# Optimization experiments

Hardware: AMD Instinct MI355X
Metric: run time of the kernel (lower is better)

The kernel has to match this reference:

```python
import jax, jax.numpy as jnp
import numpy as np

# Physical constants of the optics model (angstrom units)
WAVELENGTH = 0.025  # 200 kV electrons
DR = 0.2            # object pixel size
DZ = 10.0           # slice distance
NZ, NY, NX = 8, 512, 512
K = 256
NMODES = 4
M = 128  # detector / probe patch size
EPS = 1e-10


def _propagator_kernel():
    # Fresnel angular-spectrum transfer function, fft-shifted frequency grid
    fy = jnp.fft.fftfreq(M, d=DR).astype(jnp.float32)
    fx = jnp.fft.fftfreq(M, d=DR).astype(jnp.float32)
    f2 = fy[:, None] ** 2 + fx[None, :] ** 2  # (M, M)
    phase = -jnp.pi * WAVELENGTH * DZ * f2
    return jnp.exp(1j * phase.astype(jnp.float32))  # complex64 (M, M)


def setup_inputs() -> dict:
    key = jax.random.key(0)
    k1, k2, k3, k4 = jax.random.split(key, 4)
    V = 0.1 * jax.random.normal(k1, (NZ, NY, NX), dtype=jnp.float32)
    probe_re = jax.random.normal(k2, (NMODES, M, M), dtype=jnp.float32)
    probe_im = jax.random.normal(k3, (NMODES, M, M), dtype=jnp.float32)
    positions = jax.random.randint(k4, (K, 2), 0, NY - M).astype(jnp.int64)
    return {"V": V, "probe_re": probe_re, "probe_im": probe_im, "positions": positions}


def _forward(V, probe_re, probe_im, positions):
    # transmission function per slice: T = exp(i V)  (NZ, NY, NX) complex64
    T = jnp.exp(1j * V)
    pos = positions.astype(jnp.int32)

    # position-indexed crop: (K, NZ, M, M) -> (NZ, K, M, M)
    def crop_one(p):
        return jax.lax.dynamic_slice(T, (jnp.int32(0), p[0], p[1]), (NZ, M, M))

    patches = jax.vmap(crop_one)(pos)            # (K, NZ, M, M)
    patches = jnp.transpose(patches, (1, 0, 2, 3))  # (NZ, K, M, M)

    probe = (probe_re + 1j * probe_im)           # (Nmodes, M, M)
    waves = jnp.broadcast_to(probe[:, None, :, :], (NMODES, K, M, M))

    H = _propagator_kernel()                     # (M, M)

    def step(w, patch):
        w = patch[None] * w                      # transmit through slice
        w = jnp.fft.ifft2(jnp.fft.fft2(w) * H)   # angular-spectrum propagation
        return w, None

    waves, _ = jax.lax.scan(step, waves, patches[:-1])
    waves = waves * patches[-1][None]            # last slice, no propagation after

    # far-field intensity, incoherent sum over probe modes -> amplitudes
    psi_f = jnp.fft.fft2(waves, norm="ortho")    # (Nmodes, K, M, M)
    amp = jnp.sqrt(EPS + jnp.sum(jnp.abs(psi_f) ** 2, axis=0))  # (K, M, M)
    return amp


def reference(V, probe_re, probe_im, positions):
    return _forward(V, probe_re, probe_im, positions)
```

## Files before the change

kernel.cpp:

```cpp
#include <hip/hip_runtime.h>
#include <math.h>

namespace {

constexpr int TNZ = 8, TNY = 512, TNX = 512, TM = 128;
constexpr int PITCH = 129;
constexpr float F0 = 1.0f / (TM * 0.2f);
constexpr float PK = -3.14159265358979323846f * 0.025f * 10.0f;
constexpr float PKF = PK * F0 * F0;
constexpr float INV_N2 = 1.0f / (TM * TM);
constexpr float EPSV = 1e-10f;
constexpr float PIF = 3.14159265358979323846f;
constexpr float RT2H = 0.70710678118654752440f;

typedef float v2 __attribute__((ext_vector_type(2)));
__device__ __forceinline__ v2 mk2(float x, float y) {
  v2 r; r.x = x; r.y = y; return r;
}

template <int I> struct Ic { static constexpr int v = I; };
template <int I, int N, typename F>
__device__ __forceinline__ void u_impl(F&& f) {
  if constexpr (I < N) { f(Ic<I>{}); u_impl<I + 1, N>(f); }
}
template <int N, typename F>
__device__ __forceinline__ void u_for(F&& f) { u_impl<0, N>(f); }

__device__ __forceinline__ v2 cmul(v2 a, v2 b) {
  v2 p = a.xx * b;
  return __builtin_elementwise_fma(mk2(-a.y, a.y), b.yx, p);
}
__device__ __forceinline__ v2 cmulc(v2 a, v2 b) {
  v2 p = a.xx * mk2(b.x, -b.y);
  return __builtin_elementwise_fma(a.yy, b.yx, p);
}
__device__ __forceinline__ v2 fma2(float sg, v2 mine, v2 oth) {
  return __builtin_elementwise_fma(mk2(sg, sg), mine, oth);
}
template <int CTRL>
__device__ __forceinline__ float dppf(float v) {
  return __int_as_float(
      __builtin_amdgcn_mov_dpp(__float_as_int(v), CTRL, 0xF, 0xF, true));
}
template <int M>
__device__ __forceinline__ v2 shdpp(v2 v) {
  constexpr int CTRL = (M == 1) ? 0xB1 : 0x4E;
  return mk2(dppf<CTRL>(v.x), dppf<CTRL>(v.y));
}
template <int M>
__device__ __forceinline__ v2 shswz(v2 v) {
  constexpr int PAT = (M << 10) | 0x1F;
  return mk2(
      __int_as_float(__builtin_amdgcn_ds_swizzle(__float_as_int(v.x), PAT)),
      __int_as_float(__builtin_amdgcn_ds_swizzle(__float_as_int(v.y), PAT)));
}
__device__ __forceinline__ int rev7(int n) {
  return ((n & 1) << 6) | ((n & 2) << 4) | ((n & 4) << 2) | (n & 8) |
         ((n & 16) >> 2) | ((n & 32) >> 4) | ((n & 64) >> 6);
}
constexpr int crev3(int i) { return ((i & 1) << 2) | (i & 2) | ((i & 4) >> 2); }

template <int i> __device__ __forceinline__ v2 mulW8(v2 t) {
  if constexpr (i == 0) return t;
  else if constexpr (i == 1) return (t + mk2(t.y, -t.x)) * RT2H;
  else if constexpr (i == 2) return mk2(t.y, -t.x);
  else return (mk2(t.y, -t.x) - t) * RT2H;
}
template <int i> __device__ __forceinline__ v2 mulW8c(v2 t) {
  if constexpr (i == 0) return t;
  else if constexpr (i == 1) return (t + mk2(-t.y, t.x)) * RT2H;
  else if constexpr (i == 2) return mk2(-t.y, t.x);
  else return (mk2(-t.y, t.x) - t) * RT2H;
}

struct Tw8 {
  v2 wq128, wq64, wq32;
  v2 ws8, ws4, ws2;
  float sg8, sg4, sg2, sg1;
};

__device__ __forceinline__ void dif8(v2 (&X)[8], const Tw8& T) {
  u_for<4>([&](auto I) {
    constexpr int i = I.v;
    v2 A = X[i], B = X[i + 4];
    X[i] = A + B;
    X[i + 4] = mulW8<i>(cmul(A - B, T.wq128));
  });
  u_for<4>([&](auto I) {
    constexpr int g = (I.v >> 1) * 4 + (I.v & 1);
    v2 A = X[g], B = X[g + 2];
    X[g] = A + B;
    v2 d = cmul(A - B, T.wq64);
    X[g + 2] = (g & 1) ? mk2(d.y, -d.x) : d;
  });
  u_for<4>([&](auto I) {
    constexpr int e = I.v * 2;
    v2 A = X[e], B = X[e + 1];
    X[e] = A + B;
    X[e + 1] = cmul(A - B, T.wq32);
  });
  u_for<8>([&](auto I) {
    constexpr int i = I.v;
    v2 o = shswz<8>(X[i]);
    X[i] = cmul(fma2(T.sg8, X[i], o), T.ws8);
  });
  u_for<8>([&](auto I) {
    constexpr int i = I.v;
    v2 o = shswz<4>(X[i]);
    X[i] = cmul(fma2(T.sg4, X[i], o), T.ws4);
  });
  u_for<8>([&](auto I) {
    constexpr int i = I.v;
    v2 o = shdpp<2>(X[i]);
    X[i] = cmul(fma2(T.sg2, X[i], o), T.ws2);
  });
  u_for<8>([&](auto I) {
    constexpr int i = I.v;
    v2 o = shdpp<1>(X[i]);
    X[i] = fma2(T.sg1, X[i], o);
  });
}

__device__ __forceinline__ void dit8(v2 (&X)[8], const Tw8& T) {
  u_for<8>([&](auto I) {
    constexpr int i = I.v;
    v2 o = shdpp<1>(X[i]);
    X[i] = fma2(T.sg1, X[i], o);
  });
  u_for<8>([&](auto I) {
    constexpr int i = I.v;
    v2 u = cmulc(X[i], T.ws2);
    v2 o = shdpp<2>(u);
    X[i] = fma2(T.sg2, u, o);
  });
  u_for<8>([&](auto I) {
    constexpr int i = I.v;
    v2 u = cmulc(X[i], T.ws4);
    v2 o = shswz<4>(u);
    X[i] = fma2(T.sg4, u, o);
  });
  u_for<8>([&](auto I) {
    constexpr int i = I.v;
    v2 u = cmulc(X[i], T.ws8);
    v2 o = shswz<8>(u);
    X[i] = fma2(T.sg8, u, o);
  });
  u_for<4>([&](auto I) {
    constexpr int e = I.v * 2;
    v2 A = X[e];
    v2 t = cmulc(X[e + 1], T.wq32);
    X[e] = A + t;
    X[e + 1] = A - t;
  });
  u_for<4>([&](auto I) {
    constexpr int g = (I.v >> 1) * 4 + (I.v & 1);
    v2 A = X[g];
    v2 t0 = cmulc(X[g + 2], T.wq64);
    v2 t = (g & 1) ? mk2(-t0.y, t0.x) : t0;
    X[g] = A + t;
    X[g + 2] = A - t;
  });
  u_for<4>([&](auto I) {
    constexpr int i = I.v;
    v2 A = X[i];
    v2 t = mulW8c<i>(cmulc(X[i + 4], T.wq128));
    X[i] = A + t;
    X[i + 4] = A - t;
  });
}

template <bool PRE>
__global__ __launch_bounds__(1024)
void msp_mode(const float* __restrict__ V, const v2* __restrict__ Texp,
              const float* __restrict__ Pre, const float* __restrict__ Pim,
              const int* __restrict__ pos, float* __restrict__ out) {
  __shared__ v2 fld[TM * PITCH];
  __shared__ v2 hyb[TM];
  __shared__ v2 hxb[TM];

  const int t = threadIdx.x;
  const int k = blockIdx.x >> 2;
  const int m = blockIdx.x & 3;
  const int q = t & 15;
  const int gg = t >> 4;

  Tw8 T;
  float s, c;
  const float qf = (float)q;
  __sincosf(-PIF * qf / 64.0f, &s, &c);  T.wq128 = mk2(c, s);
  __sincosf(-PIF * qf / 32.0f, &s, &c);  T.wq64  = mk2(c, s);
  __sincosf(-PIF * qf / 16.0f, &s, &c);  T.wq32  = mk2(c, s);
  if (q & 8) { __sincosf(-PIF * (float)(q & 7) / 8.0f, &s, &c); T.ws8 = mk2(c, s); }
  else T.ws8 = mk2(1.f, 0.f);
  if (q & 4) { __sincosf(-PIF * (float)(q & 3) / 4.0f, &s, &c); T.ws4 = mk2(c, s); }
  else T.ws4 = mk2(1.f, 0.f);
  T.ws2 = (q & 2) ? ((q & 1) ? mk2(0.f, -1.f) : mk2(1.f, 0.f)) : mk2(1.f, 0.f);
  T.sg8 = (q & 8) ? -1.f : 1.f;
  T.sg4 = (q & 4) ? -1.f : 1.f;
  T.sg2 = (q & 2) ? -1.f : 1.f;
  T.sg1 = (q & 1) ? -1.f : 1.f;

  const int rev4q =
      ((q & 1) << 3) | ((q & 2) << 1) | ((q & 4) >> 1) | ((q & 8) >> 3);

  if (t < TM) {
    const int qq = t & 15, ii = t >> 4;
    const int r4 = ((qq & 1) << 3) | ((qq & 2) << 1) | ((qq & 4) >> 1) |
                   ((qq & 8) >> 3);
    const int ky = 8 * r4 + crev3(ii);
    const int iy = ky - ((ky & 64) ? 128 : 0);
    float s0, c0;
    __sincosf(PKF * (float)(iy * iy), &s0, &c0);
    hyb[t] = mk2(c0, s0);
    const int kx = rev7(t);
    const int ixf = kx - ((kx & 64) ? 128 : 0);
    __sincosf(PKF * (float)(ixf * ixf), &s0, &c0);
    hxb[t] = mk2(c0 * INV_N2, s0 * INV_N2);
  }

  const int p0 = pos[2 * k];
  const int p1 = pos[2 * k + 1];

#pragma unroll 1
  for (int h = 0; h < 2; ++h) {
    const int y = gg + 64 * h;
    const float* pr = Pre + (m * TM + y) * TM + q;
    const float* pi = Pim + (m * TM + y) * TM + q;
    u_for<8>([&](auto I) {
      constexpr int i = I.v;
      fld[y * PITCH + q + 16 * i] = mk2(pr[16 * i], pi[16 * i]);
    });
  }
  __syncthreads();

#pragma unroll 1
  for (int z = 0; z < TNZ; ++z) {
#pragma unroll 1
    for (int h = 0; h < 2; ++h) {
      const int y = gg + 64 * h;
      v2 X[8];
      u_for<8>([&](auto I) { X[I.v] = fld[y * PITCH + q + 16 * I.v]; });
      if (z > 0) dit8(X, T);
      const int off = ((z * TNY) + (p0 + y)) * TNX + p1 + q;
      if constexpr (PRE) {
        const v2* tb = Texp + off;
        u_for<8>([&](auto I) { X[I.v] = cmul(X[I.v], tb[16 * I.v]); });
      } else {
        const float* vb = V + off;
        u_for<8>([&](auto I) {
          constexpr int i = I.v;
          float v = vb[16 * i];
          float sv, cv;
          __sincosf(v, &sv, &cv);
          X[i] = cmul(X[i], mk2(cv, sv));
        });
      }
      dif8(X, T);
      u_for<8>([&](auto I) { fld[y * PITCH + q + 16 * I.v] = X[I.v]; });
    }
    __syncthreads();

    const bool last = (z == TNZ - 1);
#pragma unroll 1
    for (int h = 0; h < 2; ++h) {
      const int cc = gg + 64 * h;
      v2 X[8];
      u_for<8>([&](auto I) { X[I.v] = fld[(q + 16 * I.v) * PITCH + cc]; });
      dif8(X, T);
      if (!last) {
        const v2 hxv = hxb[cc];
        u_for<8>([&](auto I) {
          constexpr int i = I.v;
          X[i] = cmul(cmul(X[i], hyb[16 * i + q]), hxv);
        });
        dit8(X, T);
        u_for<8>([&](auto I) { fld[(q + 16 * I.v) * PITCH + cc] = X[I.v]; });
      } else {
        float* fldf = reinterpret_cast<float*>(fld);
        const int kxn = rev7(cc) ^ rev4q;
        u_for<8>([&](auto I) {
          constexpr int i = I.v;
          const int ky = 8 * rev4q + crev3(i);
          float v = fmaf(X[i].x, X[i].x, X[i].y * X[i].y);
          fldf[ky * (2 * PITCH) + kxn] = v;
        });
      }
    }
    __syncthreads();
  }

  const float* fldf = reinterpret_cast<const float*>(fld);
  float* ob = out + k * (TM * TM);
#pragma unroll
  for (int ii = 0; ii < 16; ++ii) {
    const int idx = t + 1024 * ii;
    const int ky = idx >> 7, kx = idx & 127;
    const int kxn = kx ^ ((ky >> 3) & 15);
    atomicAdd(&ob[idx], fldf[ky * (2 * PITCH) + kxn]);
  }
}

__global__ __launch_bounds__(256) void texp_k(const float* __restrict__ V,
                                              v2* __restrict__ Texp, int n) {
  const int i = blockIdx.x * 256 + threadIdx.x;
  if (i < n) {
    float s, c;
    __sincosf(V[i], &s, &c);
    Texp[i] = mk2(c, s);
  }
}

__global__ __launch_bounds__(256) void zero_k(float4* __restrict__ p, int n4) {
  const int i = blockIdx.x * 256 + threadIdx.x;
  if (i < n4) p[i] = make_float4(0.f, 0.f, 0.f, 0.f);
}

__global__ __launch_bounds__(256) void sqrt_k(float* __restrict__ p, int n) {
  const int i = blockIdx.x * 256 + threadIdx.x;
  if (i < n) p[i] = sqrtf(EPSV + p[i] * INV_N2);
}

}

extern "C" void kernel_launch(void* const* d_in, const int* in_sizes, int n_in,
                              void* d_out, int out_size, void* d_ws, size_t ws_size,
                              hipStream_t stream) {
  (void)in_sizes; (void)n_in;
  const float* V = (const float*)d_in[0];
  const float* Pre = (const float*)d_in[1];
  const float* Pim = (const float*)d_in[2];
  const int* pos = (const int*)d_in[3];
  float* out = (float*)d_out;
  const int n = out_size;
  const int n4 = n >> 2;
  zero_k<<<dim3((n4 + 255) / 256), dim3(256), 0, stream>>>((float4*)out, n4);

  const int nT = TNZ * TNY * TNX;
  const size_t texp_bytes = (size_t)nT * sizeof(v2);
  if (ws_size >= texp_bytes) {
    v2* Texp = (v2*)d_ws;
    texp_k<<<dim3((nT + 255) / 256), dim3(256), 0, stream>>>(V, Texp, nT);
    msp_mode<true><<<dim3(1024), dim3(1024), 0, stream>>>(V, Texp, Pre, Pim,
                                                          pos, out);
  } else {
    msp_mode<false><<<dim3(1024), dim3(1024), 0, stream>>>(V, nullptr, Pre,
                                                           Pim, pos, out);
  }
  sqrt_k<<<dim3((n + 255) / 256), dim3(256), 0, stream>>>(out, n);
}
```

Measured before the change: 532.3 us.

## Loop probe modes inside one block and fuse zeroing and sqrt epilogue

Each block now handles one scan position and loops over all four probe modes. Far-field intensities are accumulated in per-thread registers instead of being atomically added to global memory. The separate zero-fill and sqrt kernels are removed, and the block writes the final amplitude directly. This cuts two kernel launches, the global atomics and an extra pass over the output. In exchange the grid shrinks from 1024 to 256 blocks, and the 16 accumulator floats add register pressure at 1024 threads per block.

```diff
diff --git a/kernel.cpp b/kernel.cpp
--- a/kernel.cpp
+++ b/kernel.cpp
@@ -171,16 +171,15 @@
 
 template <bool PRE>
 __global__ __launch_bounds__(1024)
-void msp_mode(const float* __restrict__ V, const v2* __restrict__ Texp,
-              const float* __restrict__ Pre, const float* __restrict__ Pim,
-              const int* __restrict__ pos, float* __restrict__ out) {
+void msp_k(const float* __restrict__ V, const v2* __restrict__ Texp,
+           const float* __restrict__ Pre, const float* __restrict__ Pim,
+           const int* __restrict__ pos, float* __restrict__ out) {
   __shared__ v2 fld[TM * PITCH];
   __shared__ v2 hyb[TM];
   __shared__ v2 hxb[TM];
 
   const int t = threadIdx.x;
-  const int k = blockIdx.x >> 2;
-  const int m = blockIdx.x & 3;
+  const int k = blockIdx.x;
   const int q = t & 15;
   const int gg = t >> 4;
 
@@ -221,82 +220,98 @@
   const int p0 = pos[2 * k];
   const int p1 = pos[2 * k + 1];
 
+  v2 acc[8];
+  u_for<8>([&](auto I) { acc[I.v] = mk2(0.f, 0.f); });
+
+#pragma unroll 1
+  for (int m = 0; m < 4; ++m) {
+#pragma unroll 1
+    for (int h = 0; h < 2; ++h) {
+      const int y = gg + 64 * h;
+      const float* pr = Pre + (m * TM + y) * TM + q;
+      const float* pi = Pim + (m * TM + y) * TM + q;
+      u_for<8>([&](auto I) {
+        constexpr int i = I.v;
+        fld[y * PITCH + q + 16 * i] = mk2(pr[16 * i], pi[16 * i]);
+      });
+    }
+    __syncthreads();
+
+#pragma unroll 1
+    for (int z = 0; z < TNZ; ++z) {
+#pragma unroll 1
+      for (int h = 0; h < 2; ++h) {
+        const int y = gg + 64 * h;
+        v2 X[8];
+        u_for<8>([&](auto I) { X[I.v] = fld[y * PITCH + q + 16 * I.v]; });
+        if (z > 0) dit8(X, T);
+        const int off = ((z * TNY) + (p0 + y)) * TNX + p1 + q;
+        if constexpr (PRE) {
+          const v2* tb = Texp + off;
+          u_for<8>([&](auto I) { X[I.v] = cmul(X[I.v], tb[16 * I.v]); });
+        } else {
+          const float* vb = V + off;
+          u_for<8>([&](auto I) {
+            constexpr int i = I.v;
+            float v = vb[16 * i];
+            float sv, cv;
+            __sincosf(v, &sv, &cv);
+            X[i] = cmul(X[i], mk2(cv, sv));
+          });
+        }
+        dif8(X, T);
+        u_for<8>([&](auto I) { fld[y * PITCH + q + 16 * I.v] = X[I.v]; });
+      }
+      __syncthreads();
+
+      const bool last = (z == TNZ - 1);
+#pragma unroll 1
+      for (int h = 0; h < 2; ++h) {
+        const int cc = gg + 64 * h;
+        v2 X[8];
+        u_for<8>([&](auto I) { X[I.v] = fld[(q + 16 * I.v) * PITCH + cc]; });
+        dif8(X, T);
+        if (!last) {
+          const v2 hxv = hxb[cc];
+          u_for<8>([&](auto I) {
+            constexpr int i = I.v;
+            X[i] = cmul(cmul(X[i], hyb[16 * i + q]), hxv);
+          });
+          dit8(X, T);
+          u_for<8>([&](auto I) { fld[(q + 16 * I.v) * PITCH + cc] = X[I.v]; });
+        } else {
+          u_for<8>([&](auto I) {
+            constexpr int i = I.v;
+            float v = fmaf(X[i].x, X[i].x, X[i].y * X[i].y);
+            if (h == 0) acc[i].x += v; else acc[i].y += v;
+          });
+        }
+      }
+      __syncthreads();
+    }
+  }
+
+  float* fldf = reinterpret_cast<float*>(fld);
 #pragma unroll 1
   for (int h = 0; h < 2; ++h) {
-    const int y = gg + 64 * h;
-    const float* pr = Pre + (m * TM + y) * TM + q;
-    const float* pi = Pim + (m * TM + y) * TM + q;
+    const int cc = gg + 64 * h;
+    const int kxn = rev7(cc) ^ rev4q;
     u_for<8>([&](auto I) {
       constexpr int i = I.v;
-      fld[y * PITCH + q + 16 * i] = mk2(pr[16 * i], pi[16 * i]);
+      const int ky = 8 * rev4q + crev3(i);
+      fldf[ky * (2 * PITCH) + kxn] = (h == 0) ? acc[i].x : acc[i].y;
     });
   }
   __syncthreads();
 
-#pragma unroll 1
-  for (int z = 0; z < TNZ; ++z) {
-#pragma unroll 1
-    for (int h = 0; h < 2; ++h) {
-      const int y = gg + 64 * h;
-      v2 X[8];
-      u_for<8>([&](auto I) { X[I.v] = fld[y * PITCH + q + 16 * I.v]; });
-      if (z > 0) dit8(X, T);
-      const int off = ((z * TNY) + (p0 + y)) * TNX + p1 + q;
-      if constexpr (PRE) {
-        const v2* tb = Texp + off;
-        u_for<8>([&](auto I) { X[I.v] = cmul(X[I.v], tb[16 * I.v]); });
-      } else {
-        const float* vb = V + off;
-        u_for<8>([&](auto I) {
-          constexpr int i = I.v;
-          float v = vb[16 * i];
-          float sv, cv;
-          __sincosf(v, &sv, &cv);
-          X[i] = cmul(X[i], mk2(cv, sv));
-        });
-      }
-      dif8(X, T);
-      u_for<8>([&](auto I) { fld[y * PITCH + q + 16 * I.v] = X[I.v]; });
-    }
-    __syncthreads();
-
-    const bool last = (z == TNZ - 1);
-#pragma unroll 1
-    for (int h = 0; h < 2; ++h) {
-      const int cc = gg + 64 * h;
-      v2 X[8];
-      u_for<8>([&](auto I) { X[I.v] = fld[(q + 16 * I.v) * PITCH + cc]; });
-      dif8(X, T);
-      if (!last) {
-        const v2 hxv = hxb[cc];
-        u_for<8>([&](auto I) {
-          constexpr int i = I.v;
-          X[i] = cmul(cmul(X[i], hyb[16 * i + q]), hxv);
-        });
-        dit8(X, T);
-        u_for<8>([&](auto I) { fld[(q + 16 * I.v) * PITCH + cc] = X[I.v]; });
-      } else {
-        float* fldf = reinterpret_cast<float*>(fld);
-        const int kxn = rev7(cc) ^ rev4q;
-        u_for<8>([&](auto I) {
-          constexpr int i = I.v;
-          const int ky = 8 * rev4q + crev3(i);
-          float v = fmaf(X[i].x, X[i].x, X[i].y * X[i].y);
-          fldf[ky * (2 * PITCH) + kxn] = v;
-        });
-      }
-    }
-    __syncthreads();
-  }
-
-  const float* fldf = reinterpret_cast<const float*>(fld);
+  const float* cfldf = reinterpret_cast<const float*>(fld);
   float* ob = out + k * (TM * TM);
 #pragma unroll
   for (int ii = 0; ii < 16; ++ii) {
     const int idx = t + 1024 * ii;
     const int ky = idx >> 7, kx = idx & 127;
     const int kxn = kx ^ ((ky >> 3) & 15);
-    atomicAdd(&ob[idx], fldf[ky * (2 * PITCH) + kxn]);
+    ob[idx] = sqrtf(EPSV + cfldf[ky * (2 * PITCH) + kxn] * INV_N2);
   }
 }
 
@@ -310,41 +325,27 @@
   }
 }
 
-__global__ __launch_bounds__(256) void zero_k(float4* __restrict__ p, int n4) {
-  const int i = blockIdx.x * 256 + threadIdx.x;
-  if (i < n4) p[i] = make_float4(0.f, 0.f, 0.f, 0.f);
-}
-
-__global__ __launch_bounds__(256) void sqrt_k(float* __restrict__ p, int n) {
-  const int i = blockIdx.x * 256 + threadIdx.x;
-  if (i < n) p[i] = sqrtf(EPSV + p[i] * INV_N2);
-}
-
 }
 
 extern "C" void kernel_launch(void* const* d_in, const int* in_sizes, int n_in,
                               void* d_out, int out_size, void* d_ws, size_t ws_size,
                               hipStream_t stream) {
-  (void)in_sizes; (void)n_in;
+  (void)in_sizes; (void)n_in; (void)out_size;
   const float* V = (const float*)d_in[0];
   const float* Pre = (const float*)d_in[1];
   const float* Pim = (const float*)d_in[2];
   const int* pos = (const int*)d_in[3];
   float* out = (float*)d_out;
-  const int n = out_size;
-  const int n4 = n >> 2;
-  zero_k<<<dim3((n4 + 255) / 256), dim3(256), 0, stream>>>((float4*)out, n4);
 
   const int nT = TNZ * TNY * TNX;
   const size_t texp_bytes = (size_t)nT * sizeof(v2);
   if (ws_size >= texp_bytes) {
     v2* Texp = (v2*)d_ws;
     texp_k<<<dim3((nT + 255) / 256), dim3(256), 0, stream>>>(V, Texp, nT);
-    msp_mode<true><<<dim3(1024), dim3(1024), 0, stream>>>(V, Texp, Pre, Pim,
-                                                          pos, out);
+    msp_k<true><<<dim3(256), dim3(1024), 0, stream>>>(V, Texp, Pre, Pim, pos,
+                                                      out);
   } else {
-    msp_mode<false><<<dim3(1024), dim3(1024), 0, stream>>>(V, nullptr, Pre,
-                                                           Pim, pos, out);
-  }
-  sqrt_k<<<dim3((n + 255) / 256), dim3(256), 0, stream>>>(out, n);
-}
+    msp_k<false><<<dim3(256), dim3(1024), 0, stream>>>(V, nullptr, Pre, Pim,
+                                                       pos, out);
+  }
+}
```

Result: slower. 577.2 us (+8.4%).
